# Kernel tuning notes

Measured on AMD Instinct MI355X. Metric: run time of the kernel, lower is better.

The kernel has to match this reference:

```python
import jax, jax.numpy as jnp
import numpy as np
import math

INF = 10000000000.0
D_KEY = 128
SCALE = math.sqrt(D_KEY)


def setup_inputs() -> dict:
    key = jax.random.key(0)
    kq, kk, kv = jax.random.split(key, 3)
    B, S, D = 16, 2048, D_KEY
    return {
        "query": jax.random.normal(kq, (B, S, D), dtype=jnp.float32),
        "key": jax.random.normal(kk, (B, S, D), dtype=jnp.float32),
        "value": jax.random.normal(kv, (B, S, D), dtype=jnp.float32),
    }


def reference(query, key, value):
    # dot_products: [B, Sq, Sk]
    scores = jnp.einsum("bqd,bkd->bqk", query, key)
    S = key.shape[1]
    # NOTE: original subtracts the INF upper-triangular mask BEFORE dividing
    # by sqrt(d_key); replicate that order faithfully.
    tri = jnp.triu(jnp.full((S, S), INF, dtype=scores.dtype), k=1)
    scores = scores - tri[None, :, :]
    attn = jax.nn.softmax(scores / SCALE, axis=-1)
    # dropout with p=0.0 is identity
    return jnp.einsum("bqk,bkd->bqd", attn, value)
```

## Files before the change

### kernel.cpp

```cpp
#include <hip/hip_runtime.h>
#include <math.h>

#define S_LEN  2048
#define D_HEAD 128
#define QBLK   64
#define KVBLK  64
#define NWAVES 4
#define BATCH  16
#define NKVT   (S_LEN / KVBLK)
#define TILE_SH 8192

typedef __attribute__((ext_vector_type(4))) float f32x4;
typedef __attribute__((ext_vector_type(8))) short short8;

__device__ __forceinline__ unsigned short f2bf(float x) {
    union { float f; unsigned u; } v; v.f = x;
    unsigned r = v.u + 0x7fffu + ((v.u >> 16) & 1u);
    return (unsigned short)(r >> 16);
}
__device__ __forceinline__ float bf2f(unsigned short h) {
    union { unsigned u; float f; } v; v.u = ((unsigned)h) << 16;
    return v.f;
}
__device__ __forceinline__ unsigned pack2(unsigned short a, unsigned short b) {
    return (unsigned)a | ((unsigned)b << 16);
}
__device__ __forceinline__ unsigned cvtpk(float lo, float hi) {
    unsigned r;
    asm("v_cvt_pk_bf16_f32 %0, %1, %2" : "=v"(r) : "v"(lo), "v"(hi));
    return r;
}
__device__ __forceinline__ void gld16(const void* g, void* l) {
    __builtin_amdgcn_global_load_lds(
        (const __attribute__((address_space(1))) void*)g,
        (__attribute__((address_space(3))) void*)l, 16, 0, 0);
}
template<int N> __device__ __forceinline__ void wait_vm() {
    asm volatile("s_waitcnt vmcnt(%0)" :: "i"(N) : "memory");
}
__device__ __forceinline__ void barrier() {
    __builtin_amdgcn_sched_barrier(0);
    __builtin_amdgcn_s_barrier();
    __builtin_amdgcn_sched_barrier(0);
}

__global__ __launch_bounds__(256) void prep(const float* __restrict__ K,
                                            const float* __restrict__ V,
                                            unsigned short* __restrict__ Kp,
                                            unsigned short* __restrict__ Vp)
{
    const int tid = threadIdx.x;
    const int bid = blockIdx.x;
    const int b = bid >> 5, t = bid & 31;
    const size_t ibase = (size_t)b * S_LEN * D_HEAD + (size_t)t * KVBLK * D_HEAD;
    unsigned short* ko = Kp + (size_t)bid * TILE_SH;
    unsigned short* vo = Vp + (size_t)bid * TILE_SH;

    #pragma unroll
    for (int c = 0; c < 4; ++c) {
        int i  = c * 256 + tid;
        int k  = i >> 4;
        int d8 = ((i & 15) * 8) ^ ((k & 7) << 3);
        const float* sp = K + ibase + (size_t)k * D_HEAD + d8;
        float4 a = *(const float4*)sp;
        float4 bb = *(const float4*)(sp + 4);
        uint4 u = { pack2(f2bf(a.x),f2bf(a.y)),  pack2(f2bf(a.z),f2bf(a.w)),
                    pack2(f2bf(bb.x),f2bf(bb.y)),pack2(f2bf(bb.z),f2bf(bb.w)) };
        *(uint4*)(ko + i * 8) = u;
    }

    __shared__ unsigned short Vb[KVBLK][D_HEAD + 2];
    {
        const int r  = tid >> 2;
        const int c0 = (tid & 3) * 32;
        const float* sp = V + ibase + (size_t)r * D_HEAD + c0;
        #pragma unroll
        for (int i = 0; i < 8; ++i) {
            float4 x = *(const float4*)(sp + i * 4);
            Vb[r][c0+i*4+0] = f2bf(x.x); Vb[r][c0+i*4+1] = f2bf(x.y);
            Vb[r][c0+i*4+2] = f2bf(x.z); Vb[r][c0+i*4+3] = f2bf(x.w);
        }
    }
    __syncthreads();
    #pragma unroll
    for (int c = 0; c < 4; ++c) {
        int i   = c * 256 + tid;
        int d   = i >> 3;
        int kk0 = ((i & 7) * 8) ^ ((d & 7) << 3);
        unsigned short h[8];
        #pragma unroll
        for (int j = 0; j < 8; ++j) h[j] = Vb[kk0 + j][d];
        uint4 u = { pack2(h[0],h[1]), pack2(h[2],h[3]), pack2(h[4],h[5]), pack2(h[6],h[7]) };
        *(uint4*)(vo + i * 8) = u;
    }
}

template<int MODE>
__global__ __launch_bounds__(256, 4)
void attn_fwd(const float* __restrict__ Qg, const unsigned short* __restrict__ Kp,
              const unsigned short* __restrict__ Vp, float* __restrict__ Og,
              unsigned short* __restrict__ Po, float* __restrict__ Ml)
{
    constexpr float CSC = 0.12751744f;
    const int tid  = threadIdx.x;
    const int lane = tid & 63;
    const int w    = tid >> 6;
    const int bid  = blockIdx.x;

    int b, qb0, lo0, n0, qb1 = -1, n1 = 0, pslot = -1;
    if (MODE == 0) {
        b = bid & 15;
        const int rank = bid >> 4;
        qb0 = (rank < 16) ? (31 - rank) : (rank - 16);
        lo0 = 0; n0 = qb0 + 1;
    } else {
        const int o = bid >> 4;
        b = bid & 15;
        if (o < 8) {
            qb0 = o;      lo0 = 0; n0 = qb0 + 1;
            qb1 = 15 - o; n1 = qb1 + 1;
        } else {
            const int t = o - 8;
            qb0 = 31 - (t >> 1);
            const int n = qb0 + 1, h = (n + 1) >> 1, half = t & 1;
            lo0 = half ? h : 0;
            n0  = half ? (n - h) : h;
            pslot = b * 32 + t;
        }
    }
    const int nt = n0 + n1;
    const int qc = lane & 15;
    const int g  = lane >> 4;

    __shared__ __align__(16) unsigned short Klds[TILE_SH];
    __shared__ __align__(16) unsigned short Vlds[TILE_SH];
    __shared__ __align__(16) unsigned short Plds[NWAVES][16 * KVBLK];

    const size_t base = (size_t)b * S_LEN * D_HEAD;
    const int tb = b * NKVT;

    short8 qf[4];
    auto load_q = [&](int qbx) {
        const int q0wx = qbx * QBLK + w * 16;
        const float* qp = Qg + base + (size_t)(q0wx + qc) * D_HEAD + g * 8;
        #pragma unroll
        for (int db = 0; db < 4; ++db) {
            float4 x0 = *(const float4*)(qp + db * 32);
            float4 x1 = *(const float4*)(qp + db * 32 + 4);
            float tt[8] = {x0.x, x0.y, x0.z, x0.w, x1.x, x1.y, x1.z, x1.w};
            short8 f;
            #pragma unroll
            for (int j = 0; j < 8; ++j) f[j] = (short)f2bf(tt[j] * CSC);
            qf[db] = f;
        }
    };

    auto stage_K = [&](int t) {
        const unsigned short* ks = Kp + (size_t)(tb + t) * TILE_SH + w * 2048 + lane * 8;
        #pragma unroll
        for (int ii = 0; ii < 4; ++ii) gld16(ks + ii * 512, &Klds[w * 2048 + ii * 512]);
    };
    auto stage_V = [&](int t) {
        const unsigned short* vs = Vp + (size_t)(tb + t) * TILE_SH + w * 2048 + lane * 8;
        #pragma unroll
        for (int ii = 0; ii < 4; ++ii) gld16(vs + ii * 512, &Vlds[w * 2048 + ii * 512]);
    };

    f32x4 o[8] = {};
    float m = -1e30f, lsum = 0.f;

    auto epi_direct = [&](int qbx) {
        float ls = lsum;
        ls += __shfl_xor(ls, 16);
        ls += __shfl_xor(ls, 32);
        float linv = 1.0f / ls;
        float li[4];
        #pragma unroll
        for (int r = 0; r < 4; ++r) li[r] = __shfl(linv, g * 4 + r);
        const int q0wx = qbx * QBLK + w * 16;
        #pragma unroll
        for (int db = 0; db < 8; ++db)
            #pragma unroll
            for (int r = 0; r < 4; ++r)
                Og[base + (size_t)(q0wx + g * 4 + r) * D_HEAD + db * 16 + qc] = o[db][r] * li[r];
    };

    int qb_c = qb0;
    int q0w  = qb_c * QBLK + w * 16;
    int qidx = q0w + qc;

    load_q(qb_c);
    stage_K(lo0);
    stage_V(lo0);

    for (int u = 0; u < nt; ++u) {
        const int t    = (u < n0) ? (lo0 + u) : (u - n0);
        const int kv0  = t * KVBLK;
        const bool more = (u + 1 < nt);
        const int tnxt = more ? ((u + 1 < n0) ? (lo0 + u + 1) : (u + 1 - n0)) : 0;

        wait_vm<4>();
        barrier();

        const int t16max = min(3, (q0w + 15 - kv0) >> 4);
        const int ksmax  = min(1, (q0w + 15 - kv0) >> 5);

        f32x4 st[4] = {};
        __builtin_amdgcn_s_setprio(1);
        #pragma unroll
        for (int t16 = 0; t16 < 4; ++t16) {
            if (t16 <= t16max) {
                const int kr = t16 * 16 + qc;
                const int swz = (kr & 7) << 3;
                #pragma unroll
                for (int db = 0; db < 4; ++db) {
                    short8 kf = *(const short8*)&Klds[(kr * 128 + db * 32 + g * 8) ^ swz];
                    st[t16] = __builtin_amdgcn_mfma_f32_16x16x32_bf16(kf, qf[db], st[t16], 0, 0, 0);
                }
            }
        }
        __builtin_amdgcn_s_setprio(0);

        barrier();
        if (more) stage_K(tnxt);

        float s[16];
        #pragma unroll
        for (int t16 = 0; t16 < 4; ++t16)
            #pragma unroll
            for (int r = 0; r < 4; ++r)
                s[t16*4+r] = (t16 <= t16max) ? st[t16][r] : -1e30f;

        if (kv0 + KVBLK - 1 > q0w) {
            #pragma unroll
            for (int t16 = 0; t16 < 4; ++t16)
                #pragma unroll
                for (int r = 0; r < 4; ++r)
                    if (kv0 + t16 * 16 + g * 4 + r > qidx) s[t16*4+r] = -1e30f;
        }

        float m0 = fmaxf(fmaxf(s[0],s[1]), fmaxf(s[2],s[3]));
        float m1 = fmaxf(fmaxf(s[4],s[5]), fmaxf(s[6],s[7]));
        float m2 = fmaxf(fmaxf(s[8],s[9]), fmaxf(s[10],s[11]));
        float m3 = fmaxf(fmaxf(s[12],s[13]), fmaxf(s[14],s[15]));
        float mx = fmaxf(fmaxf(m0,m1), fmaxf(m2,m3));

        if (__any(mx > m + 8.0f)) {
            mx = fmaxf(mx, __shfl_xor(mx, 16));
            mx = fmaxf(mx, __shfl_xor(mx, 32));
            float mnew = fmaxf(m, mx);
            float alpha = exp2f(m - mnew);
            m = mnew;
            lsum *= alpha;
            float a_o[4];
            #pragma unroll
            for (int r = 0; r < 4; ++r) a_o[r] = __shfl(alpha, g * 4 + r);
            #pragma unroll
            for (int db = 0; db < 8; ++db)
                #pragma unroll
                for (int r = 0; r < 4; ++r) o[db][r] *= a_o[r];
        }

        float p[16];
        #pragma unroll
        for (int ii = 0; ii < 16; ++ii) p[ii] = exp2f(s[ii] - m);
        float r0 = (p[0]+p[1]) + (p[2]+p[3]);
        float r1 = (p[4]+p[5]) + (p[6]+p[7]);
        float r2 = (p[8]+p[9]) + (p[10]+p[11]);
        float r3 = (p[12]+p[13]) + (p[14]+p[15]);
        lsum += (r0+r1) + (r2+r3);

        if (more) wait_vm<4>(); else wait_vm<0>();
        barrier();

        const int pswz = (qc & 7) << 3;
        #pragma unroll
        for (int t16 = 0; t16 < 4; ++t16) {
            uint2 uu = { cvtpk(p[t16*4+0], p[t16*4+1]), cvtpk(p[t16*4+2], p[t16*4+3]) };
            *(uint2*)&Plds[w][(qc * 64 + t16 * 16 + g * 4) ^ pswz] = uu;
        }

        __builtin_amdgcn_s_setprio(1);
        #pragma unroll
        for (int ks = 0; ks < 2; ++ks) {
            if (ks <= ksmax) {
                short8 pa = *(const short8*)&Plds[w][(qc * 64 + ks * 32 + g * 8) ^ pswz];
                #pragma unroll
                for (int db = 0; db < 8; ++db) {
                    const int d = db * 16 + qc;
                    short8 vf = *(const short8*)&Vlds[(d * 64 + ks * 32 + g * 8) ^ ((d & 7) << 3)];
                    o[db] = __builtin_amdgcn_mfma_f32_16x16x32_bf16(pa, vf, o[db], 0, 0, 0);
                }
            }
        }
        __builtin_amdgcn_s_setprio(0);

        barrier();
        if (more) stage_V(tnxt);

        if (MODE == 1 && n1 > 0 && u == n0 - 1) {
            epi_direct(qb_c);
            qb_c = qb1;
            q0w  = qb_c * QBLK + w * 16;
            qidx = q0w + qc;
            load_q(qb_c);
            #pragma unroll
            for (int db = 0; db < 8; ++db) o[db] = (f32x4){0.f, 0.f, 0.f, 0.f};
            m = -1e30f; lsum = 0.f;
        }
    }

    if (MODE == 1 && pslot >= 0) {
        float ls = lsum;
        ls += __shfl_xor(ls, 16);
        ls += __shfl_xor(ls, 32);
        unsigned short* po = Po + (size_t)pslot * (QBLK * D_HEAD);
        #pragma unroll
        for (int db = 0; db < 8; ++db)
            #pragma unroll
            for (int r = 0; r < 4; ++r)
                po[(w * 16 + g * 4 + r) * D_HEAD + db * 16 + qc] = f2bf(o[db][r]);
        if (g == 0) {
            float* ml = Ml + (size_t)pslot * (QBLK * 2);
            ml[(w * 16 + qc) * 2 + 0] = m;
            ml[(w * 16 + qc) * 2 + 1] = ls;
        }
    } else {
        epi_direct(qb_c);
    }
}

__global__ __launch_bounds__(256)
void combine(const unsigned short* __restrict__ Po, const float* __restrict__ Ml,
             float* __restrict__ Og)
{
    const int z   = blockIdx.x;
    const int b   = z & 15;
    const int qb  = 16 + (z >> 4);
    const int tid = threadIdx.x;
    const int row = tid >> 2;
    const int c0  = (tid & 3) * 32;

    const int pA = b * 32 + 2 * (31 - qb);
    const int pB = pA + 1;

    const float* mlA = Ml + (size_t)pA * (QBLK * 2);
    const float* mlB = Ml + (size_t)pB * (QBLK * 2);
    const float mA = mlA[row*2], lA = mlA[row*2+1];
    const float mB = mlB[row*2], lB = mlB[row*2+1];
    const float M  = fmaxf(mA, mB);
    const float aA = exp2f(mA - M), aB = exp2f(mB - M);
    const float rd = 1.0f / (aA * lA + aB * lB);

    const unsigned short* poA = Po + (size_t)pA * (QBLK * D_HEAD) + row * D_HEAD + c0;
    const unsigned short* poB = Po + (size_t)pB * (QBLK * D_HEAD) + row * D_HEAD + c0;
    float* op = Og + (size_t)b * S_LEN * D_HEAD + (size_t)(qb * QBLK + row) * D_HEAD + c0;

    #pragma unroll
    for (int j = 0; j < 4; ++j) {
        uint4 ua = *(const uint4*)(poA + j * 8);
        uint4 ub = *(const uint4*)(poB + j * 8);
        const unsigned short* ha = (const unsigned short*)&ua;
        const unsigned short* hb = (const unsigned short*)&ub;
        float4 o0, o1;
        o0.x = (aA*bf2f(ha[0]) + aB*bf2f(hb[0])) * rd;
        o0.y = (aA*bf2f(ha[1]) + aB*bf2f(hb[1])) * rd;
        o0.z = (aA*bf2f(ha[2]) + aB*bf2f(hb[2])) * rd;
        o0.w = (aA*bf2f(ha[3]) + aB*bf2f(hb[3])) * rd;
        o1.x = (aA*bf2f(ha[4]) + aB*bf2f(hb[4])) * rd;
        o1.y = (aA*bf2f(ha[5]) + aB*bf2f(hb[5])) * rd;
        o1.z = (aA*bf2f(ha[6]) + aB*bf2f(hb[6])) * rd;
        o1.w = (aA*bf2f(ha[7]) + aB*bf2f(hb[7])) * rd;
        *(float4*)(op + j * 8)     = o0;
        *(float4*)(op + j * 8 + 4) = o1;
    }
}

extern "C" void kernel_launch(void* const* d_in, const int* in_sizes, int n_in,
                              void* d_out, int out_size, void* d_ws, size_t ws_size,
                              hipStream_t stream) {
    const float* Q = (const float*)d_in[0];
    const float* K = (const float*)d_in[1];
    const float* V = (const float*)d_in[2];
    float* O = (float*)d_out;

    const size_t tile_elems = (size_t)BATCH * NKVT * TILE_SH;
    unsigned short* Kp = (unsigned short*)d_ws;
    unsigned short* Vp = Kp + tile_elems;
    unsigned short* Po = Vp + tile_elems;
    float*          Mlp = (float*)(Po + (size_t)512 * QBLK * D_HEAD);
    const size_t need_bytes = (char*)(Mlp + (size_t)512 * QBLK * 2) - (char*)d_ws;

    prep<<<dim3(BATCH * NKVT), dim3(256), 0, stream>>>(K, V, Kp, Vp);
    if (ws_size >= need_bytes) {
        attn_fwd<1><<<dim3(640), dim3(256), 0, stream>>>(Q, Kp, Vp, O, Po, Mlp);
        combine<<<dim3(256), dim3(256), 0, stream>>>(Po, Mlp, O);
    } else {
        attn_fwd<0><<<dim3(512), dim3(256), 0, stream>>>(Q, Kp, Vp, O, nullptr, nullptr);
    }
}
```

Measured before the change: 71.05 us.

## Pair mirrored query blocks in 512-thread blocks sharing KV tiles, split KV parity

Replaces the old work split (short/long query-block pairing plus split-KV for the longest blocks) with a new kernel. Each 512-thread block handles two mirrored query blocks (p and 31-p) that share the same staged K/V tiles, and each pair is split into even and odd KV tiles across two blocks. All 32 query blocks now produce partial outputs that a combine kernel merges, aiming for balanced per-block work and fewer K/V loads per query block. The cost is a doubled partial-output workspace, a combine pass over the whole output, and waves in the low-block half that sit idle on tiles beyond their causal range.

```diff
diff --git a/kernel.cpp b/kernel.cpp
--- a/kernel.cpp
+++ b/kernel.cpp
@@ -5,7 +5,6 @@
 #define D_HEAD 128
 #define QBLK   64
 #define KVBLK  64
-#define NWAVES 4
 #define BATCH  16
 #define NKVT   (S_LEN / KVBLK)
 #define TILE_SH 8192
@@ -95,54 +94,55 @@
     }
 }
 
-template<int MODE>
-__global__ __launch_bounds__(256, 4)
-void attn_fwd(const float* __restrict__ Qg, const unsigned short* __restrict__ Kp,
-              const unsigned short* __restrict__ Vp, float* __restrict__ Og,
-              unsigned short* __restrict__ Po, float* __restrict__ Ml)
+__global__ __launch_bounds__(512, 4)
+void attn_paired(const float* __restrict__ Qg, const unsigned short* __restrict__ Kp,
+                 const unsigned short* __restrict__ Vp,
+                 unsigned short* __restrict__ Po, float* __restrict__ Ml)
 {
     constexpr float CSC = 0.12751744f;
     const int tid  = threadIdx.x;
     const int lane = tid & 63;
-    const int w    = tid >> 6;
+    const int w8   = tid >> 6;
+    const int w4   = w8 & 3;
+    const bool hi  = w8 >= 4;
     const int bid  = blockIdx.x;
-
-    int b, qb0, lo0, n0, qb1 = -1, n1 = 0, pslot = -1;
-    if (MODE == 0) {
-        b = bid & 15;
-        const int rank = bid >> 4;
-        qb0 = (rank < 16) ? (31 - rank) : (rank - 16);
-        lo0 = 0; n0 = qb0 + 1;
-    } else {
-        const int o = bid >> 4;
-        b = bid & 15;
-        if (o < 8) {
-            qb0 = o;      lo0 = 0; n0 = qb0 + 1;
-            qb1 = 15 - o; n1 = qb1 + 1;
-        } else {
-            const int t = o - 8;
-            qb0 = 31 - (t >> 1);
-            const int n = qb0 + 1, h = (n + 1) >> 1, half = t & 1;
-            lo0 = half ? h : 0;
-            n0  = half ? (n - h) : h;
-            pslot = b * 32 + t;
-        }
-    }
-    const int nt = n0 + n1;
-    const int qc = lane & 15;
-    const int g  = lane >> 4;
+    const int b    = bid & 15;
+    const int o    = bid >> 4;
+    const int j    = (o < 16) ? o : (47 - o);
+    const int p    = j >> 1, ci = j & 1;
+    const int L    = 32 - p;
+    const int len  = (L - ci + 1) >> 1;
+
+    const int qbw  = hi ? (31 - p) : p;
+    const int q0w  = qbw * QBLK + w4 * 16;
+    const int qc   = lane & 15;
+    const int g    = lane >> 4;
+    const int qidx = q0w + qc;
 
     __shared__ __align__(16) unsigned short Klds[TILE_SH];
     __shared__ __align__(16) unsigned short Vlds[TILE_SH];
-    __shared__ __align__(16) unsigned short Plds[NWAVES][16 * KVBLK];
+    __shared__ __align__(16) unsigned short Plds[8][16 * KVBLK];
 
     const size_t base = (size_t)b * S_LEN * D_HEAD;
     const int tb = b * NKVT;
 
+    auto stage_K = [&](int t) {
+        const unsigned short* ks = Kp + (size_t)(tb + t) * TILE_SH + w8 * 512 + lane * 8;
+        gld16(ks,        &Klds[w8 * 512 + lane * 8]);
+        gld16(ks + 4096, &Klds[4096 + w8 * 512 + lane * 8]);
+    };
+    auto stage_V = [&](int t) {
+        const unsigned short* vs = Vp + (size_t)(tb + t) * TILE_SH + w8 * 512 + lane * 8;
+        gld16(vs,        &Vlds[w8 * 512 + lane * 8]);
+        gld16(vs + 4096, &Vlds[4096 + w8 * 512 + lane * 8]);
+    };
+
+    stage_K(ci);
+    stage_V(ci);
+
     short8 qf[4];
-    auto load_q = [&](int qbx) {
-        const int q0wx = qbx * QBLK + w * 16;
-        const float* qp = Qg + base + (size_t)(q0wx + qc) * D_HEAD + g * 8;
+    {
+        const float* qp = Qg + base + (size_t)(q0w + qc) * D_HEAD + g * 8;
         #pragma unroll
         for (int db = 0; db < 4; ++db) {
             float4 x0 = *(const float4*)(qp + db * 32);
@@ -150,183 +150,139 @@
             float tt[8] = {x0.x, x0.y, x0.z, x0.w, x1.x, x1.y, x1.z, x1.w};
             short8 f;
             #pragma unroll
-            for (int j = 0; j < 8; ++j) f[j] = (short)f2bf(tt[j] * CSC);
+            for (int jj = 0; jj < 8; ++jj) f[jj] = (short)f2bf(tt[jj] * CSC);
             qf[db] = f;
         }
-    };
-
-    auto stage_K = [&](int t) {
-        const unsigned short* ks = Kp + (size_t)(tb + t) * TILE_SH + w * 2048 + lane * 8;
-        #pragma unroll
-        for (int ii = 0; ii < 4; ++ii) gld16(ks + ii * 512, &Klds[w * 2048 + ii * 512]);
-    };
-    auto stage_V = [&](int t) {
-        const unsigned short* vs = Vp + (size_t)(tb + t) * TILE_SH + w * 2048 + lane * 8;
-        #pragma unroll
-        for (int ii = 0; ii < 4; ++ii) gld16(vs + ii * 512, &Vlds[w * 2048 + ii * 512]);
-    };
-
-    f32x4 o[8] = {};
+    }
+
+    f32x4 acc[8] = {};
     float m = -1e30f, lsum = 0.f;
 
-    auto epi_direct = [&](int qbx) {
-        float ls = lsum;
-        ls += __shfl_xor(ls, 16);
-        ls += __shfl_xor(ls, 32);
-        float linv = 1.0f / ls;
-        float li[4];
-        #pragma unroll
-        for (int r = 0; r < 4; ++r) li[r] = __shfl(linv, g * 4 + r);
-        const int q0wx = qbx * QBLK + w * 16;
-        #pragma unroll
-        for (int db = 0; db < 8; ++db)
-            #pragma unroll
-            for (int r = 0; r < 4; ++r)
-                Og[base + (size_t)(q0wx + g * 4 + r) * D_HEAD + db * 16 + qc] = o[db][r] * li[r];
-    };
-
-    int qb_c = qb0;
-    int q0w  = qb_c * QBLK + w * 16;
-    int qidx = q0w + qc;
-
-    load_q(qb_c);
-    stage_K(lo0);
-    stage_V(lo0);
-
-    for (int u = 0; u < nt; ++u) {
-        const int t    = (u < n0) ? (lo0 + u) : (u - n0);
-        const int kv0  = t * KVBLK;
-        const bool more = (u + 1 < nt);
-        const int tnxt = more ? ((u + 1 < n0) ? (lo0 + u + 1) : (u + 1 - n0)) : 0;
-
-        wait_vm<4>();
+    for (int i = 0; i < len; ++i) {
+        const int t   = ci + 2 * i;
+        const int kv0 = t * KVBLK;
+        const bool more = (i + 1 < len);
+
+        wait_vm<2>();
         barrier();
 
         const int t16max = min(3, (q0w + 15 - kv0) >> 4);
         const int ksmax  = min(1, (q0w + 15 - kv0) >> 5);
+        const bool active = t16max >= 0;
 
         f32x4 st[4] = {};
-        __builtin_amdgcn_s_setprio(1);
-        #pragma unroll
-        for (int t16 = 0; t16 < 4; ++t16) {
-            if (t16 <= t16max) {
-                const int kr = t16 * 16 + qc;
-                const int swz = (kr & 7) << 3;
-                #pragma unroll
-                for (int db = 0; db < 4; ++db) {
-                    short8 kf = *(const short8*)&Klds[(kr * 128 + db * 32 + g * 8) ^ swz];
-                    st[t16] = __builtin_amdgcn_mfma_f32_16x16x32_bf16(kf, qf[db], st[t16], 0, 0, 0);
+        if (active) {
+            __builtin_amdgcn_s_setprio(1);
+            #pragma unroll
+            for (int t16 = 0; t16 < 4; ++t16) {
+                if (t16 <= t16max) {
+                    const int kr = t16 * 16 + qc;
+                    const int swz = (kr & 7) << 3;
+                    #pragma unroll
+                    for (int db = 0; db < 4; ++db) {
+                        short8 kf = *(const short8*)&Klds[(kr * 128 + db * 32 + g * 8) ^ swz];
+                        st[t16] = __builtin_amdgcn_mfma_f32_16x16x32_bf16(kf, qf[db], st[t16], 0, 0, 0);
+                    }
                 }
             }
-        }
-        __builtin_amdgcn_s_setprio(0);
-
-        barrier();
-        if (more) stage_K(tnxt);
-
-        float s[16];
-        #pragma unroll
-        for (int t16 = 0; t16 < 4; ++t16)
-            #pragma unroll
-            for (int r = 0; r < 4; ++r)
-                s[t16*4+r] = (t16 <= t16max) ? st[t16][r] : -1e30f;
-
-        if (kv0 + KVBLK - 1 > q0w) {
+            __builtin_amdgcn_s_setprio(0);
+        }
+
+        barrier();
+        if (more) stage_K(t + 2);
+
+        float p16[16];
+        if (active) {
+            float s[16];
             #pragma unroll
             for (int t16 = 0; t16 < 4; ++t16)
                 #pragma unroll
                 for (int r = 0; r < 4; ++r)
-                    if (kv0 + t16 * 16 + g * 4 + r > qidx) s[t16*4+r] = -1e30f;
-        }
-
-        float m0 = fmaxf(fmaxf(s[0],s[1]), fmaxf(s[2],s[3]));
-        float m1 = fmaxf(fmaxf(s[4],s[5]), fmaxf(s[6],s[7]));
-        float m2 = fmaxf(fmaxf(s[8],s[9]), fmaxf(s[10],s[11]));
-        float m3 = fmaxf(fmaxf(s[12],s[13]), fmaxf(s[14],s[15]));
-        float mx = fmaxf(fmaxf(m0,m1), fmaxf(m2,m3));
-
-        if (__any(mx > m + 8.0f)) {
-            mx = fmaxf(mx, __shfl_xor(mx, 16));
-            mx = fmaxf(mx, __shfl_xor(mx, 32));
-            float mnew = fmaxf(m, mx);
-            float alpha = exp2f(m - mnew);
-            m = mnew;
-            lsum *= alpha;
-            float a_o[4];
-            #pragma unroll
-            for (int r = 0; r < 4; ++r) a_o[r] = __shfl(alpha, g * 4 + r);
-            #pragma unroll
-            for (int db = 0; db < 8; ++db)
-                #pragma unroll
-                for (int r = 0; r < 4; ++r) o[db][r] *= a_o[r];
-        }
-
-        float p[16];
-        #pragma unroll
-        for (int ii = 0; ii < 16; ++ii) p[ii] = exp2f(s[ii] - m);
-        float r0 = (p[0]+p[1]) + (p[2]+p[3]);
-        float r1 = (p[4]+p[5]) + (p[6]+p[7]);
-        float r2 = (p[8]+p[9]) + (p[10]+p[11]);
-        float r3 = (p[12]+p[13]) + (p[14]+p[15]);
-        lsum += (r0+r1) + (r2+r3);
-
-        if (more) wait_vm<4>(); else wait_vm<0>();
-        barrier();
-
-        const int pswz = (qc & 7) << 3;
-        #pragma unroll
-        for (int t16 = 0; t16 < 4; ++t16) {
-            uint2 uu = { cvtpk(p[t16*4+0], p[t16*4+1]), cvtpk(p[t16*4+2], p[t16*4+3]) };
-            *(uint2*)&Plds[w][(qc * 64 + t16 * 16 + g * 4) ^ pswz] = uu;
-        }
-
-        __builtin_amdgcn_s_setprio(1);
-        #pragma unroll
-        for (int ks = 0; ks < 2; ++ks) {
-            if (ks <= ksmax) {
-                short8 pa = *(const short8*)&Plds[w][(qc * 64 + ks * 32 + g * 8) ^ pswz];
-                #pragma unroll
-                for (int db = 0; db < 8; ++db) {
-                    const int d = db * 16 + qc;
-                    short8 vf = *(const short8*)&Vlds[(d * 64 + ks * 32 + g * 8) ^ ((d & 7) << 3)];
-                    o[db] = __builtin_amdgcn_mfma_f32_16x16x32_bf16(pa, vf, o[db], 0, 0, 0);
+                    s[t16*4+r] = (t16 <= t16max) ? st[t16][r] : -1e30f;
+
+            if (kv0 + KVBLK - 1 > q0w) {
+                #pragma unroll
+                for (int t16 = 0; t16 < 4; ++t16)
+                    #pragma unroll
+                    for (int r = 0; r < 4; ++r)
+                        if (kv0 + t16 * 16 + g * 4 + r > qidx) s[t16*4+r] = -1e30f;
+            }
+
+            float m0 = fmaxf(fmaxf(s[0],s[1]), fmaxf(s[2],s[3]));
+            float m1 = fmaxf(fmaxf(s[4],s[5]), fmaxf(s[6],s[7]));
+            float m2 = fmaxf(fmaxf(s[8],s[9]), fmaxf(s[10],s[11]));
+            float m3 = fmaxf(fmaxf(s[12],s[13]), fmaxf(s[14],s[15]));
+            float mx = fmaxf(fmaxf(m0,m1), fmaxf(m2,m3));
+
+            if (__any(mx > m + 8.0f)) {
+                mx = fmaxf(mx, __shfl_xor(mx, 16));
+                mx = fmaxf(mx, __shfl_xor(mx, 32));
+                float mnew = fmaxf(m, mx);
+                float alpha = exp2f(m - mnew);
+                m = mnew;
+                lsum *= alpha;
+                float a_o[4];
+                #pragma unroll
+                for (int r = 0; r < 4; ++r) a_o[r] = __shfl(alpha, g * 4 + r);
+                #pragma unroll
+                for (int db = 0; db < 8; ++db)
+                    #pragma unroll
+                    for (int r = 0; r < 4; ++r) acc[db][r] *= a_o[r];
+            }
+
+            #pragma unroll
+            for (int ii = 0; ii < 16; ++ii) p16[ii] = exp2f(s[ii] - m);
+            float r0 = (p16[0]+p16[1]) + (p16[2]+p16[3]);
+            float r1 = (p16[4]+p16[5]) + (p16[6]+p16[7]);
+            float r2 = (p16[8]+p16[9]) + (p16[10]+p16[11]);
+            float r3 = (p16[12]+p16[13]) + (p16[14]+p16[15]);
+            lsum += (r0+r1) + (r2+r3);
+        }
+
+        if (more) wait_vm<2>(); else wait_vm<0>();
+        barrier();
+
+        if (active) {
+            const int pswz = (qc & 7) << 3;
+            #pragma unroll
+            for (int t16 = 0; t16 < 4; ++t16) {
+                uint2 uu = { cvtpk(p16[t16*4+0], p16[t16*4+1]), cvtpk(p16[t16*4+2], p16[t16*4+3]) };
+                *(uint2*)&Plds[w8][(qc * 64 + t16 * 16 + g * 4) ^ pswz] = uu;
+            }
+            __builtin_amdgcn_s_setprio(1);
+            #pragma unroll
+            for (int ks = 0; ks < 2; ++ks) {
+                if (ks <= ksmax) {
+                    short8 pa = *(const short8*)&Plds[w8][(qc * 64 + ks * 32 + g * 8) ^ pswz];
+                    #pragma unroll
+                    for (int db = 0; db < 8; ++db) {
+                        const int d = db * 16 + qc;
+                        short8 vf = *(const short8*)&Vlds[(d * 64 + ks * 32 + g * 8) ^ ((d & 7) << 3)];
+                        acc[db] = __builtin_amdgcn_mfma_f32_16x16x32_bf16(pa, vf, acc[db], 0, 0, 0);
+                    }
                 }
             }
-        }
-        __builtin_amdgcn_s_setprio(0);
-
-        barrier();
-        if (more) stage_V(tnxt);
-
-        if (MODE == 1 && n1 > 0 && u == n0 - 1) {
-            epi_direct(qb_c);
-            qb_c = qb1;
-            q0w  = qb_c * QBLK + w * 16;
-            qidx = q0w + qc;
-            load_q(qb_c);
-            #pragma unroll
-            for (int db = 0; db < 8; ++db) o[db] = (f32x4){0.f, 0.f, 0.f, 0.f};
-            m = -1e30f; lsum = 0.f;
-        }
-    }
-
-    if (MODE == 1 && pslot >= 0) {
-        float ls = lsum;
-        ls += __shfl_xor(ls, 16);
-        ls += __shfl_xor(ls, 32);
-        unsigned short* po = Po + (size_t)pslot * (QBLK * D_HEAD);
-        #pragma unroll
-        for (int db = 0; db < 8; ++db)
-            #pragma unroll
-            for (int r = 0; r < 4; ++r)
-                po[(w * 16 + g * 4 + r) * D_HEAD + db * 16 + qc] = f2bf(o[db][r]);
-        if (g == 0) {
-            float* ml = Ml + (size_t)pslot * (QBLK * 2);
-            ml[(w * 16 + qc) * 2 + 0] = m;
-            ml[(w * 16 + qc) * 2 + 1] = ls;
-        }
-    } else {
-        epi_direct(qb_c);
+            __builtin_amdgcn_s_setprio(0);
+        }
+
+        barrier();
+        if (more) stage_V(t + 2);
+    }
+
+    lsum += __shfl_xor(lsum, 16);
+    lsum += __shfl_xor(lsum, 32);
+
+    const int pslot = ((((b << 4) | p) * 2 + ci) << 1) + (hi ? 1 : 0);
+    unsigned short* po = Po + (size_t)pslot * (QBLK * D_HEAD);
+    #pragma unroll
+    for (int db = 0; db < 8; ++db)
+        #pragma unroll
+        for (int r = 0; r < 4; ++r)
+            po[(w4 * 16 + g * 4 + r) * D_HEAD + db * 16 + qc] = f2bf(acc[db][r]);
+    if (g == 0) {
+        float* ml = Ml + (size_t)pslot * (QBLK * 2);
+        ml[(w4 * 16 + qc) * 2 + 0] = m;
+        ml[(w4 * 16 + qc) * 2 + 1] = lsum;
     }
 }
 
@@ -336,13 +292,15 @@
 {
     const int z   = blockIdx.x;
     const int b   = z & 15;
-    const int qb  = 16 + (z >> 4);
+    const int qb  = z >> 4;
     const int tid = threadIdx.x;
     const int row = tid >> 2;
     const int c0  = (tid & 3) * 32;
 
-    const int pA = b * 32 + 2 * (31 - qb);
-    const int pB = pA + 1;
+    const int set = (qb > 15) ? 1 : 0;
+    const int p   = set ? (31 - qb) : qb;
+    const int pA  = ((((b << 4) | p) * 2 + 0) << 1) + set;
+    const int pB  = ((((b << 4) | p) * 2 + 1) << 1) + set;
 
     const float* mlA = Ml + (size_t)pA * (QBLK * 2);
     const float* mlB = Ml + (size_t)pB * (QBLK * 2);
@@ -357,9 +315,9 @@
     float* op = Og + (size_t)b * S_LEN * D_HEAD + (size_t)(qb * QBLK + row) * D_HEAD + c0;
 
     #pragma unroll
-    for (int j = 0; j < 4; ++j) {
-        uint4 ua = *(const uint4*)(poA + j * 8);
-        uint4 ub = *(const uint4*)(poB + j * 8);
+    for (int jj = 0; jj < 4; ++jj) {
+        uint4 ua = *(const uint4*)(poA + jj * 8);
+        uint4 ub = *(const uint4*)(poB + jj * 8);
         const unsigned short* ha = (const unsigned short*)&ua;
         const unsigned short* hb = (const unsigned short*)&ub;
         float4 o0, o1;
@@ -371,9 +329,175 @@
         o1.y = (aA*bf2f(ha[5]) + aB*bf2f(hb[5])) * rd;
         o1.z = (aA*bf2f(ha[6]) + aB*bf2f(hb[6])) * rd;
         o1.w = (aA*bf2f(ha[7]) + aB*bf2f(hb[7])) * rd;
-        *(float4*)(op + j * 8)     = o0;
-        *(float4*)(op + j * 8 + 4) = o1;
-    }
+        *(float4*)(op + jj * 8)     = o0;
+        *(float4*)(op + jj * 8 + 4) = o1;
+    }
+}
+
+__global__ __launch_bounds__(256, 2)
+void attn_direct(const float* __restrict__ Qg, const unsigned short* __restrict__ Kp,
+                 const unsigned short* __restrict__ Vp, float* __restrict__ Og)
+{
+    constexpr float CSC = 0.12751744f;
+    const int tid  = threadIdx.x;
+    const int lane = tid & 63;
+    const int w    = tid >> 6;
+    const int bid  = blockIdx.x;
+    const int b    = bid & 15;
+    const int rank = bid >> 4;
+    const int qb   = (rank < 16) ? (31 - rank) : (rank - 16);
+    const int q0w  = qb * QBLK + w * 16;
+    const int qc   = lane & 15;
+    const int g    = lane >> 4;
+    const int qidx = q0w + qc;
+
+    __shared__ __align__(16) unsigned short Klds[TILE_SH];
+    __shared__ __align__(16) unsigned short Vlds[TILE_SH];
+    __shared__ __align__(16) unsigned short Plds[4][16 * KVBLK];
+
+    const size_t base = (size_t)b * S_LEN * D_HEAD;
+    const int tb = b * NKVT;
+
+    auto stage_K = [&](int t) {
+        const unsigned short* ks = Kp + (size_t)(tb + t) * TILE_SH + w * 2048 + lane * 8;
+        #pragma unroll
+        for (int ii = 0; ii < 4; ++ii) gld16(ks + ii * 512, &Klds[w * 2048 + ii * 512]);
+    };
+    auto stage_V = [&](int t) {
+        const unsigned short* vs = Vp + (size_t)(tb + t) * TILE_SH + w * 2048 + lane * 8;
+        #pragma unroll
+        for (int ii = 0; ii < 4; ++ii) gld16(vs + ii * 512, &Vlds[w * 2048 + ii * 512]);
+    };
+
+    short8 qf[4];
+    {
+        const float* qp = Qg + base + (size_t)(q0w + qc) * D_HEAD + g * 8;
+        #pragma unroll
+        for (int db = 0; db < 4; ++db) {
+            float4 x0 = *(const float4*)(qp + db * 32);
+            float4 x1 = *(const float4*)(qp + db * 32 + 4);
+            float tt[8] = {x0.x, x0.y, x0.z, x0.w, x1.x, x1.y, x1.z, x1.w};
+            short8 f;
+            #pragma unroll
+            for (int jj = 0; jj < 8; ++jj) f[jj] = (short)f2bf(tt[jj] * CSC);
+            qf[db] = f;
+        }
+    }
+
+    f32x4 acc[8] = {};
+    float m = -1e30f, lsum = 0.f;
+    const int nt = qb + 1;
+
+    stage_K(0);
+    stage_V(0);
+
+    for (int t = 0; t < nt; ++t) {
+        const int kv0 = t * KVBLK;
+        const bool more = (t + 1 < nt);
+        wait_vm<4>();
+        barrier();
+
+        const int t16max = min(3, (q0w + 15 - kv0) >> 4);
+        const int ksmax  = min(1, (q0w + 15 - kv0) >> 5);
+
+        f32x4 st[4] = {};
+        __builtin_amdgcn_s_setprio(1);
+        #pragma unroll
+        for (int t16 = 0; t16 < 4; ++t16) {
+            if (t16 <= t16max) {
+                const int kr = t16 * 16 + qc;
+                const int swz = (kr & 7) << 3;
+                #pragma unroll
+                for (int db = 0; db < 4; ++db) {
+                    short8 kf = *(const short8*)&Klds[(kr * 128 + db * 32 + g * 8) ^ swz];
+                    st[t16] = __builtin_amdgcn_mfma_f32_16x16x32_bf16(kf, qf[db], st[t16], 0, 0, 0);
+                }
+            }
+        }
+        __builtin_amdgcn_s_setprio(0);
+        barrier();
+        if (more) stage_K(t + 1);
+
+        float s[16];
+        #pragma unroll
+        for (int t16 = 0; t16 < 4; ++t16)
+            #pragma unroll
+            for (int r = 0; r < 4; ++r)
+                s[t16*4+r] = (t16 <= t16max) ? st[t16][r] : -1e30f;
+        if (kv0 + KVBLK - 1 > q0w) {
+            #pragma unroll
+            for (int t16 = 0; t16 < 4; ++t16)
+                #pragma unroll
+                for (int r = 0; r < 4; ++r)
+                    if (kv0 + t16 * 16 + g * 4 + r > qidx) s[t16*4+r] = -1e30f;
+        }
+        float m0 = fmaxf(fmaxf(s[0],s[1]), fmaxf(s[2],s[3]));
+        float m1 = fmaxf(fmaxf(s[4],s[5]), fmaxf(s[6],s[7]));
+        float m2 = fmaxf(fmaxf(s[8],s[9]), fmaxf(s[10],s[11]));
+        float m3 = fmaxf(fmaxf(s[12],s[13]), fmaxf(s[14],s[15]));
+        float mx = fmaxf(fmaxf(m0,m1), fmaxf(m2,m3));
+        if (__any(mx > m + 8.0f)) {
+            mx = fmaxf(mx, __shfl_xor(mx, 16));
+            mx = fmaxf(mx, __shfl_xor(mx, 32));
+            float mnew = fmaxf(m, mx);
+            float alpha = exp2f(m - mnew);
+            m = mnew;
+            lsum *= alpha;
+            float a_o[4];
+            #pragma unroll
+            for (int r = 0; r < 4; ++r) a_o[r] = __shfl(alpha, g * 4 + r);
+            #pragma unroll
+            for (int db = 0; db < 8; ++db)
+                #pragma unroll
+                for (int r = 0; r < 4; ++r) acc[db][r] *= a_o[r];
+        }
+        float p16[16];
+        #pragma unroll
+        for (int ii = 0; ii < 16; ++ii) p16[ii] = exp2f(s[ii] - m);
+        float r0 = (p16[0]+p16[1]) + (p16[2]+p16[3]);
+        float r1 = (p16[4]+p16[5]) + (p16[6]+p16[7]);
+        float r2 = (p16[8]+p16[9]) + (p16[10]+p16[11]);
+        float r3 = (p16[12]+p16[13]) + (p16[14]+p16[15]);
+        lsum += (r0+r1) + (r2+r3);
+
+        if (more) wait_vm<4>(); else wait_vm<0>();
+        barrier();
+
+        const int pswz = (qc & 7) << 3;
+        #pragma unroll
+        for (int t16 = 0; t16 < 4; ++t16) {
+            uint2 uu = { cvtpk(p16[t16*4+0], p16[t16*4+1]), cvtpk(p16[t16*4+2], p16[t16*4+3]) };
+            *(uint2*)&Plds[w][(qc * 64 + t16 * 16 + g * 4) ^ pswz] = uu;
+        }
+        __builtin_amdgcn_s_setprio(1);
+        #pragma unroll
+        for (int ks = 0; ks < 2; ++ks) {
+            if (ks <= ksmax) {
+                short8 pa = *(const short8*)&Plds[w][(qc * 64 + ks * 32 + g * 8) ^ pswz];
+                #pragma unroll
+                for (int db = 0; db < 8; ++db) {
+                    const int d = db * 16 + qc;
+                    short8 vf = *(const short8*)&Vlds[(d * 64 + ks * 32 + g * 8) ^ ((d & 7) << 3)];
+                    acc[db] = __builtin_amdgcn_mfma_f32_16x16x32_bf16(pa, vf, acc[db], 0, 0, 0);
+                }
+            }
+        }
+        __builtin_amdgcn_s_setprio(0);
+        barrier();
+        if (more) stage_V(t + 1);
+    }
+
+    lsum += __shfl_xor(lsum, 16);
+    lsum += __shfl_xor(lsum, 32);
+    float linv = 1.0f / lsum;
+    float li[4];
+    #pragma unroll
+    for (int r = 0; r < 4; ++r) li[r] = __shfl(linv, g * 4 + r);
+    #pragma unroll
+    for (int db = 0; db < 8; ++db)
+        #pragma unroll
+        for (int r = 0; r < 4; ++r)
+            Og[base + (size_t)(q0w + g * 4 + r) * D_HEAD + db * 16 + qc] = acc[db][r] * li[r];
 }
 
 extern "C" void kernel_launch(void* const* d_in, const int* in_sizes, int n_in,
@@ -388,14 +512,14 @@
     unsigned short* Kp = (unsigned short*)d_ws;
     unsigned short* Vp = Kp + tile_elems;
     unsigned short* Po = Vp + tile_elems;
-    float*          Mlp = (float*)(Po + (size_t)512 * QBLK * D_HEAD);
-    const size_t need_bytes = (char*)(Mlp + (size_t)512 * QBLK * 2) - (char*)d_ws;
+    float*          Mlp = (float*)(Po + (size_t)1024 * QBLK * D_HEAD);
+    const size_t need_bytes = (char*)(Mlp + (size_t)1024 * QBLK * 2) - (char*)d_ws;
 
     prep<<<dim3(BATCH * NKVT), dim3(256), 0, stream>>>(K, V, Kp, Vp);
     if (ws_size >= need_bytes) {
-        attn_fwd<1><<<dim3(640), dim3(256), 0, stream>>>(Q, Kp, Vp, O, Po, Mlp);
-        combine<<<dim3(256), dim3(256), 0, stream>>>(Po, Mlp, O);
+        attn_paired<<<dim3(512), dim3(512), 0, stream>>>(Q, Kp, Vp, Po, Mlp);
+        combine<<<dim3(32 * BATCH), dim3(256), 0, stream>>>(Po, Mlp, O);
     } else {
-        attn_fwd<0><<<dim3(512), dim3(256), 0, stream>>>(Q, Kp, Vp, O, nullptr, nullptr);
-    }
-}
+        attn_direct<<<dim3(512), dim3(256), 0, stream>>>(Q, Kp, Vp, O);
+    }
+}
```

Result: slower. 85.84 us (+20.8%).
